# Kernel tuning notes

Measured on AMD Instinct MI355X. Metric: run time of the kernel, lower is better.

Reference implementation:

```python
import jax, jax.numpy as jnp
import numpy as np

B, T, N, C = 4, 2048, 8, 64
HEADS, HEAD_DIM, V_UNIT, EMBED = 8, 64, 64, 64  # N*C == HEADS*HEAD_DIM == 512


def setup_inputs() -> dict:
    key = jax.random.key(0)
    ks = jax.random.split(key, 6)
    return {
        "values": jax.random.normal(ks[0], (B, T, N, C), dtype=jnp.float32),
        "keys": jax.random.normal(ks[1], (B, T, N, C), dtype=jnp.float32),
        "queries": jax.random.normal(ks[2], (B, T, N, C), dtype=jnp.float32),
        "Wq": jax.random.normal(ks[3], (HEADS * HEAD_DIM, N * C), dtype=jnp.float32) * 0.02,
        "W_fc": jax.random.normal(ks[4], (EMBED, EMBED), dtype=jnp.float32) * 0.02,
        "b_fc": jax.random.normal(ks[5], (EMBED,), dtype=jnp.float32) * 0.02,
    }


def reference(values, keys, queries, Wq, W_fc, b_fc):
    b, t, n, c = queries.shape
    atten_dim = t  # temporal mode
    # queries: flatten N*C, project, split heads -> [B, T, H, Dh]
    q = queries.reshape(b, atten_dim, n * c) @ Wq.T
    q = q.reshape(b, atten_dim, HEADS, HEAD_DIM)
    # keys/values: only reshaped in the original forward (their Linears are unused)
    k = keys.reshape(b, atten_dim, HEADS, HEAD_DIM)
    v = values.reshape(b, atten_dim, HEADS, V_UNIT)
    # energy: [B, Tq, Tk, H]
    energy = jnp.einsum("bqhd,bkhd->bqkh", q, k)
    # diagonal-exclusion mask applied additively BEFORE scaling (as in source)
    diag = jnp.eye(atten_dim, dtype=bool)[None, :, :, None]
    energy = jnp.where(diag, jnp.float32(-1e9), energy)
    attention = jax.nn.softmax(energy / jnp.sqrt(jnp.float32(HEAD_DIM)), axis=2)
    out = jnp.einsum("bqkh,bkhd->bqhd", attention, v)  # [B, T, H, Dv]
    out = out @ W_fc.T + b_fc
    return out
```

## Files before the change

kernel.cpp:

```cpp
#include <hip/hip_runtime.h>
#include <math.h>

#define BB 4
#define TT 2048
#define NH 8
#define HD 64
#define EMB 512

typedef unsigned short u16;
typedef short short8 __attribute__((ext_vector_type(8)));
typedef float f32x4 __attribute__((ext_vector_type(4)));
typedef float f32x16 __attribute__((ext_vector_type(16)));

#define MFMA32(a,b,c) __builtin_amdgcn_mfma_f32_32x32x16_bf16((a),(b),(c),0,0,0)
#define ZERO16 (f32x16){0.f,0.f,0.f,0.f,0.f,0.f,0.f,0.f,0.f,0.f,0.f,0.f,0.f,0.f,0.f,0.f}
#define QSCALE 0.1803368801111f

#if __has_builtin(__builtin_amdgcn_exp2f)
#define EXP2(x) __builtin_amdgcn_exp2f(x)
#else
#define EXP2(x) exp2f(x)
#endif

__device__ __forceinline__ float hi_part(float a) {
    return __uint_as_float(__float_as_uint(a) & 0xffff0000u);
}
__device__ __forceinline__ unsigned pack_hi2(float a, float b) {
    return (__float_as_uint(a) >> 16) | (__float_as_uint(b) & 0xffff0000u);
}
__device__ __forceinline__ unsigned pack_lo2(float a, float b) {
    return pack_hi2(a - hi_part(a), b - hi_part(b));
}
__device__ __forceinline__ unsigned rne1(float x) {
    unsigned u = __float_as_uint(x);
    return (u + 0x7fffu + ((u >> 16) & 1u)) >> 16;
}
__device__ __forceinline__ unsigned rne2(float a, float b) {
    return rne1(a) | (rne1(b) << 16);
}
__device__ __forceinline__ void gl_lds16(const u16* g, void* l) {
    __builtin_amdgcn_global_load_lds(
        (const __attribute__((address_space(1))) unsigned int*)g,
        (__attribute__((address_space(3))) unsigned int*)l, 16, 0, 0);
}

__global__ __launch_bounds__(256, 3) void prep(
        const float* __restrict__ Aq, const float* __restrict__ Wq,
        const float* __restrict__ K,  const float* __restrict__ V,
        const float* __restrict__ Wfc,
        u16* __restrict__ Qh, u16* __restrict__ Ql,
        u16* __restrict__ Kh, u16* __restrict__ Vh,
        u16* __restrict__ Wh, u16* __restrict__ Wl) {
    __shared__ __align__(16) unsigned char sm[49152];
    const int tid = threadIdx.x;

    if (blockIdx.x < 512) {
        const int AoffH = 0, AoffL = 16384, BoffH = 32768, BoffL = 40960;
        const int lane = tid & 63, w = tid >> 6;
        const int l31 = lane & 31, hh2 = lane >> 5;
        const int qb = (blockIdx.x & 63) * 128, ob = (blockIdx.x >> 6) * 64;
        const int ar = tid >> 1, ahalf = tid & 1;
        const int br = tid >> 2, bq = tid & 3;

        const float* ap = Aq + (size_t)(qb + ar) * EMB + ahalf * 32;
        const float* bp = Wq + (size_t)(ob + br) * EMB + bq * 16;

        float4 a4[8], b4[4];
        #pragma unroll
        for (int c = 0; c < 8; c++) a4[c] = *(const float4*)(ap + 4*c);
        #pragma unroll
        for (int c = 0; c < 4; c++) b4[c] = *(const float4*)(bp + 4*c);

        f32x16 acc[2] = {ZERO16, ZERO16};

        for (int k0 = 0; k0 < EMB; k0 += 64) {
            __syncthreads();
            #pragma unroll
            for (int c = 0; c < 4; c++) {
                float4 f0 = a4[2*c], f1 = a4[2*c+1];
                uint4 hh = make_uint4(pack_hi2(f0.x,f0.y), pack_hi2(f0.z,f0.w),
                                      pack_hi2(f1.x,f1.y), pack_hi2(f1.z,f1.w));
                uint4 ll = make_uint4(pack_lo2(f0.x,f0.y), pack_lo2(f0.z,f0.w),
                                      pack_lo2(f1.x,f1.y), pack_lo2(f1.z,f1.w));
                const int phys = ((ahalf*4 + c) ^ (ar & 7)) * 16;
                *(uint4*)(sm + AoffH + ar*128 + phys) = hh;
                *(uint4*)(sm + AoffL + ar*128 + phys) = ll;
            }
            #pragma unroll
            for (int c = 0; c < 2; c++) {
                float4 f0 = b4[2*c], f1 = b4[2*c+1];
                uint4 hh = make_uint4(pack_hi2(f0.x,f0.y), pack_hi2(f0.z,f0.w),
                                      pack_hi2(f1.x,f1.y), pack_hi2(f1.z,f1.w));
                uint4 ll = make_uint4(pack_lo2(f0.x,f0.y), pack_lo2(f0.z,f0.w),
                                      pack_lo2(f1.x,f1.y), pack_lo2(f1.z,f1.w));
                const int phys = ((bq*2 + c) ^ (br & 7)) * 16;
                *(uint4*)(sm + BoffH + br*128 + phys) = hh;
                *(uint4*)(sm + BoffL + br*128 + phys) = ll;
            }
            if (k0 + 64 < EMB) {
                #pragma unroll
                for (int c = 0; c < 8; c++) a4[c] = *(const float4*)(ap + k0 + 64 + 4*c);
                #pragma unroll
                for (int c = 0; c < 4; c++) b4[c] = *(const float4*)(bp + k0 + 64 + 4*c);
            }
            __syncthreads();

            const unsigned char* arow = sm + (w*32 + l31) * 128;
            #pragma unroll
            for (int ks = 0; ks < 4; ks++) {
                const int co = (((ks*2 + hh2) ^ (l31 & 7)) * 16);
                short8 ah = *(const short8*)(arow + AoffH + co);
                short8 al = *(const short8*)(arow + AoffL + co);
                #pragma unroll
                for (int nb = 0; nb < 2; nb++) {
                    const unsigned char* brow = sm + (nb*32 + l31) * 128 + co;
                    short8 bh = *(const short8*)(brow + BoffH);
                    short8 bl = *(const short8*)(brow + BoffL);
                    acc[nb] = MFMA32(ah, bh, acc[nb]);
                    acc[nb] = MFMA32(al, bh, acc[nb]);
                    acc[nb] = MFMA32(ah, bl, acc[nb]);
                }
            }
        }

        __syncthreads();
        float* Ls = (float*)sm;
        #pragma unroll
        for (int nb = 0; nb < 2; nb++)
            #pragma unroll
            for (int rg = 0; rg < 16; rg++) {
                const int row = w*32 + (rg & 3) + 8*(rg >> 2) + 4*hh2;
                Ls[row*68 + nb*32 + l31] = acc[nb][rg] * QSCALE;
            }
        const int q = w*32 + (lane >> 1), o0 = (lane & 1) * 32;
        float v[32];
        #pragma unroll
        for (int j = 0; j < 8; j++) {
            f32x4 t = *(const f32x4*)(Ls + q*68 + o0 + 4*j);
            v[4*j]=t[0]; v[4*j+1]=t[1]; v[4*j+2]=t[2]; v[4*j+3]=t[3];
        }
        u16* qd = Qh + (size_t)(qb + q) * EMB + ob + o0;
        u16* ql = Ql + (size_t)(qb + q) * EMB + ob + o0;
        #pragma unroll
        for (int c = 0; c < 4; c++) {
            uint4 hh = make_uint4(pack_hi2(v[8*c],v[8*c+1]), pack_hi2(v[8*c+2],v[8*c+3]),
                                  pack_hi2(v[8*c+4],v[8*c+5]), pack_hi2(v[8*c+6],v[8*c+7]));
            uint4 ll = make_uint4(pack_lo2(v[8*c],v[8*c+1]), pack_lo2(v[8*c+2],v[8*c+3]),
                                  pack_lo2(v[8*c+4],v[8*c+5]), pack_lo2(v[8*c+6],v[8*c+7]));
            *(uint4*)(qd + 8*c) = hh;
            *(uint4*)(ql + 8*c) = ll;
        }
    } else {
        const int u = blockIdx.x - 512;
        const int kt0 = (u & 31) * 64, h = (u >> 5) & 7, b = u >> 8;
        float (*Vf)[68] = (float(*)[68])sm;
        const int t = tid >> 2, c0 = (tid & 3) * 16;
        {
            const float* kp = K + ((size_t)(b*TT + kt0 + t)) * EMB + h*HD + c0;
            float v[16];
            #pragma unroll
            for (int j = 0; j < 4; j++) {
                float4 f = *(const float4*)(kp + 4*j);
                v[4*j]=f.x; v[4*j+1]=f.y; v[4*j+2]=f.z; v[4*j+3]=f.w;
            }
            u16* kd = Kh + ((size_t)(b*NH + h)*TT + kt0 + t)*HD;
            #pragma unroll
            for (int half = 0; half < 2; half++) {
                const int phys = ((c0 >> 3) + half) ^ (t & 7);
                unsigned hh[4];
                #pragma unroll
                for (int j = 0; j < 4; j++)
                    hh[j] = rne2(v[half*8 + 2*j], v[half*8 + 2*j + 1]);
                *(uint4*)(kd + phys*8) = make_uint4(hh[0],hh[1],hh[2],hh[3]);
            }
        }
        {
            const float* vp = V + ((size_t)(b*TT + kt0 + t)) * EMB + h*HD + c0;
            #pragma unroll
            for (int j = 0; j < 4; j++)
                *(float4*)&Vf[t][c0 + 4*j] = *(const float4*)(vp + 4*j);
        }
        __syncthreads();
        {
            const int d = tid >> 2, t0 = (tid & 3) * 16;
            float v[16];
            #pragma unroll
            for (int i = 0; i < 16; i++) v[i] = Vf[t0 + i][d];
            u16* vd = Vh + (((size_t)(b*NH + h)*32 + (kt0 >> 6))*64 + d)*64;
            #pragma unroll
            for (int half = 0; half < 2; half++) {
                const int phys = ((t0 >> 3) + half) ^ (d & 7);
                unsigned hh[4];
                #pragma unroll
                for (int j = 0; j < 4; j++)
                    hh[j] = rne2(v[half*8 + 2*j], v[half*8 + 2*j + 1]);
                *(uint4*)(vd + phys*8) = make_uint4(hh[0],hh[1],hh[2],hh[3]);
            }
        }
        if (u == 0) {
            const int i0 = tid * 16;
            float v[16];
            #pragma unroll
            for (int j = 0; j < 4; j++) {
                float4 f = *(const float4*)(Wfc + i0 + 4*j);
                v[4*j]=f.x; v[4*j+1]=f.y; v[4*j+2]=f.z; v[4*j+3]=f.w;
            }
            unsigned hh[8], ll[8];
            #pragma unroll
            for (int j = 0; j < 8; j++) {
                hh[j] = pack_hi2(v[2*j], v[2*j+1]);
                ll[j] = pack_lo2(v[2*j], v[2*j+1]);
            }
            *(uint4*)(Wh + i0)     = make_uint4(hh[0],hh[1],hh[2],hh[3]);
            *(uint4*)(Wh + i0 + 8) = make_uint4(hh[4],hh[5],hh[6],hh[7]);
            *(uint4*)(Wl + i0)     = make_uint4(ll[0],ll[1],ll[2],ll[3]);
            *(uint4*)(Wl + i0 + 8) = make_uint4(ll[4],ll[5],ll[6],ll[7]);
        }
    }
}

__global__ __launch_bounds__(256, 3) void attn_v6(
        const u16* __restrict__ Qh, const u16* __restrict__ Ql,
        const u16* __restrict__ Kh, const u16* __restrict__ Vh,
        const u16* __restrict__ Wh, const u16* __restrict__ Wl,
        const float* __restrict__ bfc, float* __restrict__ out) {
    __shared__ __align__(16) unsigned char sm[49152];

    const int tid = threadIdx.x, lane = tid & 63, w = tid >> 6;
    const int l31 = lane & 31, hh2 = lane >> 5;
    const int s = l31 & 7, s0 = s & 1, t3 = s >> 1;
    const int qb = blockIdx.x * 128, h = blockIdx.y, b = blockIdx.z;
    const int qg = qb + w*32 + l31;
    const int rowoff = l31 * 128;

    int fo[4];
    #pragma unroll
    for (int f = 0; f < 4; f++)
        fo[f] = ((f ^ t3) << 5) | ((hh2 ^ s0) << 4);

    const size_t qo = ((size_t)(b*TT + qg)) * EMB + h*HD + hh2*8;
    short8 qfh[4], qfl[4];
    #pragma unroll
    for (int f = 0; f < 4; f++) {
        qfh[f] = *(const short8*)(Qh + qo + 16*f);
        qfl[f] = *(const short8*)(Ql + qo + 16*f);
    }

    const size_t bh = (size_t)(b*NH + h) * TT * HD;
    const u16* ssrc = ((w < 2) ? (Kh + bh) : (Vh + bh)) + (w & 1) * 2048;
    const int sdst = ((w >= 2) ? 8192 : 0) + (w & 1) * 4096;

    #pragma unroll
    for (int i = 0; i < 4; i++)
        gl_lds16(ssrc + i*512 + lane*8, sm + sdst + i*1024);
    __syncthreads();

    f32x16 co[2] = {ZERO16, ZERO16};
    float lsum = 0.f;
    const int diagTile = (qb >> 6) + (w >> 1);
    const int Poff = 32768 + w * 4096;

    for (int kt = 0; kt < 32; kt++) {
        const int cb = (kt & 1) * 16384;
        if (kt < 31) {
            const u16* src2 = ssrc + (size_t)(kt + 1) * 4096;
            unsigned char* dst2 = sm + (16384 - cb) + sdst;
            #pragma unroll
            for (int i = 0; i < 4; i++)
                gl_lds16(src2 + i*512 + lane*8, dst2 + i*1024);
        }

        f32x16 sc[2];
        #pragma unroll
        for (int kc = 0; kc < 2; kc++) {
            const unsigned char* kb = sm + cb + kc*4096 + rowoff;
            f32x16 c = ZERO16;
            #pragma unroll
            for (int f = 0; f < 4; f++) {
                short8 ah = *(const short8*)(kb + fo[f]);
                c = MFMA32(ah, qfh[f], c);
                c = MFMA32(ah, qfl[f], c);
            }
            sc[kc] = c;
        }

        if (kt == diagTile) {
            const int local = qg & 63;
            if (((local >> 2) & 1) == hh2) {
                const int reg = (local & 3) + ((local >> 3) & 3) * 4;
                if (local < 32) sc[0][reg] = -1e30f;
                else            sc[1][reg] = -1e30f;
            }
        }

        #pragma unroll
        for (int kc = 0; kc < 2; kc++)
            #pragma unroll
            for (int e = 0; e < 16; e++) {
                float p = EXP2(sc[kc][e]);
                sc[kc][e] = p;
                lsum += p;
            }

        #pragma unroll
        for (int kc = 0; kc < 2; kc++)
            #pragma unroll
            for (int rg = 0; rg < 4; rg++) {
                uint2 hh = make_uint2(pack_hi2(sc[kc][rg*4+0], sc[kc][rg*4+1]),
                                      pack_hi2(sc[kc][rg*4+2], sc[kc][rg*4+3]));
                *(uint2*)(sm + Poff + rowoff +
                          ((((kc*4 + rg) ^ s) << 4) + (hh2 << 3))) = hh;
            }

        short8 pb[4];
        #pragma unroll
        for (int f = 0; f < 4; f++)
            pb[f] = *(const short8*)(sm + Poff + rowoff + fo[f]);
        #pragma unroll
        for (int m = 0; m < 2; m++) {
            const unsigned char* vb = sm + cb + 8192 + m*4096 + rowoff;
            #pragma unroll
            for (int f = 0; f < 4; f++) {
                short8 vh = *(const short8*)(vb + fo[f]);
                co[m] = MFMA32(vh, pb[f], co[m]);
            }
        }
        __syncthreads();
    }

    lsum += __shfl_xor(lsum, 32, 64);
    const float rl = 1.f / lsum;
    const int aOffH = w * 4096, aOffL = 16384 + w * 4096;
    #pragma unroll
    for (int m = 0; m < 2; m++)
        #pragma unroll
        for (int rg = 0; rg < 4; rg++) {
            float a0 = co[m][rg*4+0]*rl, a1 = co[m][rg*4+1]*rl;
            float a2 = co[m][rg*4+2]*rl, a3 = co[m][rg*4+3]*rl;
            uint2 hh = make_uint2(pack_hi2(a0,a1), pack_hi2(a2,a3));
            uint2 ll = make_uint2(pack_lo2(a0,a1), pack_lo2(a2,a3));
            const int off = rowoff + ((((m*4 + rg) ^ s) << 4) + (hh2 << 3));
            *(uint2*)(sm + aOffH + off) = hh;
            *(uint2*)(sm + aOffL + off) = ll;
        }
    short8 abh[4], abl[4];
    #pragma unroll
    for (int f = 0; f < 4; f++) {
        abh[f] = *(const short8*)(sm + aOffH + rowoff + fo[f]);
        abl[f] = *(const short8*)(sm + aOffL + rowoff + fo[f]);
    }
    f32x16 cf[2] = {ZERO16, ZERO16};
    #pragma unroll
    for (int eh = 0; eh < 2; eh++) {
        const u16* wp  = Wh + (eh*32 + l31)*HD + hh2*8;
        const u16* wpl = Wl + (eh*32 + l31)*HD + hh2*8;
        #pragma unroll
        for (int f = 0; f < 4; f++) {
            short8 whv = *(const short8*)(wp + 16*f);
            cf[eh] = MFMA32(whv, abh[f], cf[eh]);
        }
        #pragma unroll
        for (int f = 0; f < 4; f++) {
            short8 wlv = *(const short8*)(wpl + 16*f);
            cf[eh] = MFMA32(wlv, abh[f], cf[eh]);
        }
        #pragma unroll
        for (int f = 0; f < 4; f++) {
            short8 whv = *(const short8*)(wp + 16*f);
            cf[eh] = MFMA32(whv, abl[f], cf[eh]);
        }
    }
    __syncthreads();
    float* Ls = (float*)sm;
    #pragma unroll
    for (int eh = 0; eh < 2; eh++)
        #pragma unroll
        for (int rg = 0; rg < 4; rg++) {
            const int e0 = eh*32 + rg*8 + hh2*4;
            *(f32x4*)(Ls + (w*32 + l31)*72 + e0) =
                (f32x4){cf[eh][rg*4+0], cf[eh][rg*4+1], cf[eh][rg*4+2], cf[eh][rg*4+3]};
        }
    const int q2 = w*32 + (lane >> 1), e0s = (lane & 1) * 32;
    const float* lrow = Ls + q2*72 + e0s;
    float* orow = out + ((size_t)((b*TT + qb + q2)*NH + h))*HD + e0s;
    #pragma unroll
    for (int j = 0; j < 8; j++) {
        f32x4 v = *(const f32x4*)(lrow + 4*j);
        float4 bv = *(const float4*)(bfc + e0s + 4*j);
        *(float4*)(orow + 4*j) = make_float4(v[0]+bv.x, v[1]+bv.y, v[2]+bv.z, v[3]+bv.w);
    }
}

__global__ __launch_bounds__(256) void qproj_f32(const float* __restrict__ A,
                                                 const float* __restrict__ W,
                                                 float* __restrict__ Q) {
    __shared__ float As[16][68];
    __shared__ float Ws[16][68];
    const int tid = threadIdx.x;
    const int bm = blockIdx.x * 64, bo = blockIdx.y * 64;
    const int tx = tid & 15, ty = tid >> 4;
    const int lm = tid >> 2, lk = (tid & 3) * 4;
    float acc[4][4] = {};
    for (int k0 = 0; k0 < EMB; k0 += 16) {
        float4 a4 = *(const float4*)(A + (size_t)(bm + lm) * EMB + k0 + lk);
        float4 w4 = *(const float4*)(W + (size_t)(bo + lm) * EMB + k0 + lk);
        As[lk+0][lm]=a4.x; As[lk+1][lm]=a4.y; As[lk+2][lm]=a4.z; As[lk+3][lm]=a4.w;
        Ws[lk+0][lm]=w4.x; Ws[lk+1][lm]=w4.y; Ws[lk+2][lm]=w4.z; Ws[lk+3][lm]=w4.w;
        __syncthreads();
        #pragma unroll
        for (int k = 0; k < 16; k++) {
            float a[4], ww[4];
            #pragma unroll
            for (int i = 0; i < 4; i++) a[i] = As[k][ty*4+i];
            #pragma unroll
            for (int j = 0; j < 4; j++) ww[j] = Ws[k][tx*4+j];
            #pragma unroll
            for (int i = 0; i < 4; i++)
                #pragma unroll
                for (int j = 0; j < 4; j++) acc[i][j] = fmaf(a[i], ww[j], acc[i][j]);
        }
        __syncthreads();
    }
    #pragma unroll
    for (int i = 0; i < 4; i++)
        #pragma unroll
        for (int j = 0; j < 4; j++)
            Q[(size_t)(bm + ty*4 + i) * EMB + bo + tx*4 + j] = acc[i][j];
}

__device__ __forceinline__ float rdlane(float v, int l) {
    return __uint_as_float(__builtin_amdgcn_readlane(__float_as_uint(v), l));
}

__global__ __launch_bounds__(256) void attn_valu(const float* __restrict__ qws,
                                                 const float* __restrict__ keys,
                                                 const float* __restrict__ values,
                                                 const float* __restrict__ Wfc,
                                                 const float* __restrict__ bfc,
                                                 float* __restrict__ out) {
    __shared__ float Kt[64][65];
    __shared__ float Vt[64][65];
    __shared__ float Wfs[64][64];
    __shared__ float bfs[64];
    const int tid = threadIdx.x, lane = tid & 63, wave = tid >> 6;
    const int h = blockIdx.y, b = blockIdx.z;
    const int rowBase = blockIdx.x * 32 + wave * 8;
    #pragma unroll
    for (int rep = 0; rep < 4; rep++) {
        int e4 = rep * 256 + tid;
        int e = e4 >> 4, d = (e4 & 15) * 4;
        float4 w4 = *(const float4*)(Wfc + e * 64 + d);
        Wfs[d+0][e]=w4.x; Wfs[d+1][e]=w4.y; Wfs[d+2][e]=w4.z; Wfs[d+3][e]=w4.w;
    }
    if (tid < 64) bfs[tid] = bfc[tid];
    float qreg[8];
    #pragma unroll
    for (int r = 0; r < 8; r++)
        qreg[r] = qws[(((size_t)b * TT + rowBase + r) * NH + h) * HD + lane];
    float m[8], lsum[8], acc[8];
    #pragma unroll
    for (int r = 0; r < 8; r++) { m[r] = -INFINITY; lsum[r] = 0.f; acc[r] = 0.f; }
    const float* kbase = keys   + ((size_t)b * TT * NH + h) * HD;
    const float* vbase = values + ((size_t)b * TT * NH + h) * HD;
    for (int kt0 = 0; kt0 < TT; kt0 += 64) {
        __syncthreads();
        #pragma unroll
        for (int rep = 0; rep < 4; rep++) {
            int e4 = rep * 256 + tid;
            int kr = e4 >> 4, d = (e4 & 15) * 4;
            size_t g = ((size_t)(kt0 + kr) * NH) * HD + d;
            float4 k4 = *(const float4*)(kbase + g);
            float4 v4 = *(const float4*)(vbase + g);
            Kt[kr][d+0]=k4.x; Kt[kr][d+1]=k4.y; Kt[kr][d+2]=k4.z; Kt[kr][d+3]=k4.w;
            Vt[kr][d+0]=v4.x; Vt[kr][d+1]=v4.y; Vt[kr][d+2]=v4.z; Vt[kr][d+3]=v4.w;
        }
        __syncthreads();
        float en[8];
        #pragma unroll
        for (int r = 0; r < 8; r++) en[r] = 0.f;
        #pragma unroll 16
        for (int d = 0; d < 64; d++) {
            float kv = Kt[lane][d];
            #pragma unroll
            for (int r = 0; r < 8; r++) en[r] = fmaf(rdlane(qreg[r], d), kv, en[r]);
        }
        const int key = kt0 + lane;
        float p[8], alph[8];
        #pragma unroll
        for (int r = 0; r < 8; r++) {
            float e = en[r];
            if (key == rowBase + r) e = -1e9f;
            e *= 0.125f;
            float tm = e;
            #pragma unroll
            for (int ss = 32; ss > 0; ss >>= 1) tm = fmaxf(tm, __shfl_xor(tm, ss, 64));
            float mn = fmaxf(m[r], tm);
            float pvv = __expf(e - mn);
            float ps = pvv;
            #pragma unroll
            for (int ss = 32; ss > 0; ss >>= 1) ps += __shfl_xor(ps, ss, 64);
            alph[r] = __expf(m[r] - mn);
            m[r] = mn;
            lsum[r] = lsum[r] * alph[r] + ps;
            p[r] = pvv;
        }
        #pragma unroll
        for (int r = 0; r < 8; r++) acc[r] *= alph[r];
        #pragma unroll 16
        for (int j = 0; j < 64; j++) {
            float vv = Vt[j][lane];
            #pragma unroll
            for (int r = 0; r < 8; r++) acc[r] = fmaf(rdlane(p[r], j), vv, acc[r]);
        }
    }
    #pragma unroll
    for (int r = 0; r < 8; r++) {
        float a = acc[r] / lsum[r];
        float o = bfs[lane];
        #pragma unroll 16
        for (int d = 0; d < 64; d++) o = fmaf(rdlane(a, d), Wfs[d][lane], o);
        out[(((size_t)b * TT + rowBase + r) * NH + h) * HD + lane] = o;
    }
}

extern "C" void kernel_launch(void* const* d_in, const int* in_sizes, int n_in,
                              void* d_out, int out_size, void* d_ws, size_t ws_size,
                              hipStream_t stream) {
    const float* values  = (const float*)d_in[0];
    const float* keys    = (const float*)d_in[1];
    const float* queries = (const float*)d_in[2];
    const float* Wq      = (const float*)d_in[3];
    const float* Wfc     = (const float*)d_in[4];
    const float* bfc     = (const float*)d_in[5];
    float* out = (float*)d_out;

    const size_t NE = (size_t)BB * TT * EMB;
    const size_t need = (4 * NE + 2 * 4096) * sizeof(u16);
    if (ws_size >= need) {
        u16* Qh = (u16*)d_ws;
        u16* Ql = Qh + NE;
        u16* Kh = Qh + 2*NE;
        u16* Vh = Qh + 3*NE;
        u16* Wh = Qh + 4*NE;
        u16* Wl = Wh + 4096;
        prep<<<1536, 256, 0, stream>>>(queries, Wq, keys, values, Wfc,
                                       Qh, Ql, Kh, Vh, Wh, Wl);
        attn_v6<<<dim3(TT/128, NH, BB), 256, 0, stream>>>(Qh, Ql, Kh, Vh,
                                                          Wh, Wl, bfc, out);
    } else {
        float* qws = (float*)d_ws;
        qproj_f32<<<dim3((BB*TT)/64, EMB/64), 256, 0, stream>>>(queries, Wq, qws);
        attn_valu<<<dim3(TT/32, NH, BB), 256, 0, stream>>>(qws, keys, values, Wfc, bfc, out);
    }
}
```

Baseline: 180.1 us.

## Split prep into Q-projection and K/V conversion kernels, RNE-round P

```diff
diff --git a/kernel.cpp b/kernel.cpp
--- a/kernel.cpp
+++ b/kernel.cpp
@@ -44,182 +44,187 @@
         (__attribute__((address_space(3))) unsigned int*)l, 16, 0, 0);
 }
 
-__global__ __launch_bounds__(256, 3) void prep(
-        const float* __restrict__ Aq, const float* __restrict__ Wq,
-        const float* __restrict__ K,  const float* __restrict__ V,
-        const float* __restrict__ Wfc,
-        u16* __restrict__ Qh, u16* __restrict__ Ql,
-        u16* __restrict__ Kh, u16* __restrict__ Vh,
-        u16* __restrict__ Wh, u16* __restrict__ Wl) {
+__global__ __launch_bounds__(256, 3) void qproj_pf(const float* __restrict__ Aq,
+                                                   const float* __restrict__ Wq,
+                                                   u16* __restrict__ Qh,
+                                                   u16* __restrict__ Ql) {
     __shared__ __align__(16) unsigned char sm[49152];
+    const int AoffH = 0, AoffL = 16384, BoffH = 32768, BoffL = 40960;
     const int tid = threadIdx.x;
-
-    if (blockIdx.x < 512) {
-        const int AoffH = 0, AoffL = 16384, BoffH = 32768, BoffL = 40960;
-        const int lane = tid & 63, w = tid >> 6;
-        const int l31 = lane & 31, hh2 = lane >> 5;
-        const int qb = (blockIdx.x & 63) * 128, ob = (blockIdx.x >> 6) * 64;
-        const int ar = tid >> 1, ahalf = tid & 1;
-        const int br = tid >> 2, bq = tid & 3;
-
-        const float* ap = Aq + (size_t)(qb + ar) * EMB + ahalf * 32;
-        const float* bp = Wq + (size_t)(ob + br) * EMB + bq * 16;
-
-        float4 a4[8], b4[4];
-        #pragma unroll
-        for (int c = 0; c < 8; c++) a4[c] = *(const float4*)(ap + 4*c);
-        #pragma unroll
-        for (int c = 0; c < 4; c++) b4[c] = *(const float4*)(bp + 4*c);
-
-        f32x16 acc[2] = {ZERO16, ZERO16};
-
-        for (int k0 = 0; k0 < EMB; k0 += 64) {
-            __syncthreads();
-            #pragma unroll
-            for (int c = 0; c < 4; c++) {
-                float4 f0 = a4[2*c], f1 = a4[2*c+1];
-                uint4 hh = make_uint4(pack_hi2(f0.x,f0.y), pack_hi2(f0.z,f0.w),
-                                      pack_hi2(f1.x,f1.y), pack_hi2(f1.z,f1.w));
-                uint4 ll = make_uint4(pack_lo2(f0.x,f0.y), pack_lo2(f0.z,f0.w),
-                                      pack_lo2(f1.x,f1.y), pack_lo2(f1.z,f1.w));
-                const int phys = ((ahalf*4 + c) ^ (ar & 7)) * 16;
-                *(uint4*)(sm + AoffH + ar*128 + phys) = hh;
-                *(uint4*)(sm + AoffL + ar*128 + phys) = ll;
+    const int lane = tid & 63, w = tid >> 6;
+    const int l31 = lane & 31, hh2 = lane >> 5;
+    const int qb = (blockIdx.x & 63) * 128, ob = (blockIdx.x >> 6) * 64;
+    const int ar = tid >> 1, ahalf = tid & 1;
+    const int br = tid >> 2, bq = tid & 3;
+
+    const float* ap = Aq + (size_t)(qb + ar) * EMB + ahalf * 32;
+    const float* bp = Wq + (size_t)(ob + br) * EMB + bq * 16;
+
+    float4 a4[8], b4[4];
+    #pragma unroll
+    for (int c = 0; c < 8; c++) a4[c] = *(const float4*)(ap + 4*c);
+    #pragma unroll
+    for (int c = 0; c < 4; c++) b4[c] = *(const float4*)(bp + 4*c);
+
+    f32x16 acc[2] = {ZERO16, ZERO16};
+
+    for (int k0 = 0; k0 < EMB; k0 += 64) {
+        __syncthreads();
+        #pragma unroll
+        for (int c = 0; c < 4; c++) {
+            float4 f0 = a4[2*c], f1 = a4[2*c+1];
+            uint4 hh = make_uint4(pack_hi2(f0.x,f0.y), pack_hi2(f0.z,f0.w),
+                                  pack_hi2(f1.x,f1.y), pack_hi2(f1.z,f1.w));
+            uint4 ll = make_uint4(pack_lo2(f0.x,f0.y), pack_lo2(f0.z,f0.w),
+                                  pack_lo2(f1.x,f1.y), pack_lo2(f1.z,f1.w));
+            const int phys = ((ahalf*4 + c) ^ (ar & 7)) * 16;
+            *(uint4*)(sm + AoffH + ar*128 + phys) = hh;
+            *(uint4*)(sm + AoffL + ar*128 + phys) = ll;
+        }
+        #pragma unroll
+        for (int c = 0; c < 2; c++) {
+            float4 f0 = b4[2*c], f1 = b4[2*c+1];
+            uint4 hh = make_uint4(pack_hi2(f0.x,f0.y), pack_hi2(f0.z,f0.w),
+                                  pack_hi2(f1.x,f1.y), pack_hi2(f1.z,f1.w));
+            uint4 ll = make_uint4(pack_lo2(f0.x,f0.y), pack_lo2(f0.z,f0.w),
+                                  pack_lo2(f1.x,f1.y), pack_lo2(f1.z,f1.w));
+            const int phys = ((bq*2 + c) ^ (br & 7)) * 16;
+            *(uint4*)(sm + BoffH + br*128 + phys) = hh;
+            *(uint4*)(sm + BoffL + br*128 + phys) = ll;
+        }
+        if (k0 + 64 < EMB) {
+            #pragma unroll
+            for (int c = 0; c < 8; c++) a4[c] = *(const float4*)(ap + k0 + 64 + 4*c);
+            #pragma unroll
+            for (int c = 0; c < 4; c++) b4[c] = *(const float4*)(bp + k0 + 64 + 4*c);
+        }
+        __syncthreads();
+
+        const unsigned char* arow = sm + (w*32 + l31) * 128;
+        #pragma unroll
+        for (int ks = 0; ks < 4; ks++) {
+            const int co = (((ks*2 + hh2) ^ (l31 & 7)) * 16);
+            short8 ah = *(const short8*)(arow + AoffH + co);
+            short8 al = *(const short8*)(arow + AoffL + co);
+            #pragma unroll
+            for (int nb = 0; nb < 2; nb++) {
+                const unsigned char* brow = sm + (nb*32 + l31) * 128 + co;
+                short8 bh = *(const short8*)(brow + BoffH);
+                short8 bl = *(const short8*)(brow + BoffL);
+                acc[nb] = MFMA32(ah, bh, acc[nb]);
+                acc[nb] = MFMA32(al, bh, acc[nb]);
+                acc[nb] = MFMA32(ah, bl, acc[nb]);
             }
-            #pragma unroll
-            for (int c = 0; c < 2; c++) {
-                float4 f0 = b4[2*c], f1 = b4[2*c+1];
-                uint4 hh = make_uint4(pack_hi2(f0.x,f0.y), pack_hi2(f0.z,f0.w),
-                                      pack_hi2(f1.x,f1.y), pack_hi2(f1.z,f1.w));
-                uint4 ll = make_uint4(pack_lo2(f0.x,f0.y), pack_lo2(f0.z,f0.w),
-                                      pack_lo2(f1.x,f1.y), pack_lo2(f1.z,f1.w));
-                const int phys = ((bq*2 + c) ^ (br & 7)) * 16;
-                *(uint4*)(sm + BoffH + br*128 + phys) = hh;
-                *(uint4*)(sm + BoffL + br*128 + phys) = ll;
-            }
-            if (k0 + 64 < EMB) {
-                #pragma unroll
-                for (int c = 0; c < 8; c++) a4[c] = *(const float4*)(ap + k0 + 64 + 4*c);
-                #pragma unroll
-                for (int c = 0; c < 4; c++) b4[c] = *(const float4*)(bp + k0 + 64 + 4*c);
-            }
-            __syncthreads();
-
-            const unsigned char* arow = sm + (w*32 + l31) * 128;
-            #pragma unroll
-            for (int ks = 0; ks < 4; ks++) {
-                const int co = (((ks*2 + hh2) ^ (l31 & 7)) * 16);
-                short8 ah = *(const short8*)(arow + AoffH + co);
-                short8 al = *(const short8*)(arow + AoffL + co);
-                #pragma unroll
-                for (int nb = 0; nb < 2; nb++) {
-                    const unsigned char* brow = sm + (nb*32 + l31) * 128 + co;
-                    short8 bh = *(const short8*)(brow + BoffH);
-                    short8 bl = *(const short8*)(brow + BoffL);
-                    acc[nb] = MFMA32(ah, bh, acc[nb]);
-                    acc[nb] = MFMA32(al, bh, acc[nb]);
-                    acc[nb] = MFMA32(ah, bl, acc[nb]);
-                }
-            }
-        }
-
-        __syncthreads();
-        float* Ls = (float*)sm;
-        #pragma unroll
-        for (int nb = 0; nb < 2; nb++)
-            #pragma unroll
-            for (int rg = 0; rg < 16; rg++) {
-                const int row = w*32 + (rg & 3) + 8*(rg >> 2) + 4*hh2;
-                Ls[row*68 + nb*32 + l31] = acc[nb][rg] * QSCALE;
-            }
-        const int q = w*32 + (lane >> 1), o0 = (lane & 1) * 32;
-        float v[32];
+        }
+    }
+
+    __syncthreads();
+    float* Ls = (float*)sm;
+    #pragma unroll
+    for (int nb = 0; nb < 2; nb++)
+        #pragma unroll
+        for (int rg = 0; rg < 16; rg++) {
+            const int row = w*32 + (rg & 3) + 8*(rg >> 2) + 4*hh2;
+            Ls[row*68 + nb*32 + l31] = acc[nb][rg] * QSCALE;
+        }
+    const int q = w*32 + (lane >> 1), o0 = (lane & 1) * 32;
+    float v[32];
+    #pragma unroll
+    for (int j = 0; j < 8; j++) {
+        f32x4 t = *(const f32x4*)(Ls + q*68 + o0 + 4*j);
+        v[4*j]=t[0]; v[4*j+1]=t[1]; v[4*j+2]=t[2]; v[4*j+3]=t[3];
+    }
+    u16* qd = Qh + (size_t)(qb + q) * EMB + ob + o0;
+    u16* ql = Ql + (size_t)(qb + q) * EMB + ob + o0;
+    #pragma unroll
+    for (int c = 0; c < 4; c++) {
+        uint4 hh = make_uint4(pack_hi2(v[8*c],v[8*c+1]), pack_hi2(v[8*c+2],v[8*c+3]),
+                              pack_hi2(v[8*c+4],v[8*c+5]), pack_hi2(v[8*c+6],v[8*c+7]));
+        uint4 ll = make_uint4(pack_lo2(v[8*c],v[8*c+1]), pack_lo2(v[8*c+2],v[8*c+3]),
+                              pack_lo2(v[8*c+4],v[8*c+5]), pack_lo2(v[8*c+6],v[8*c+7]));
+        *(uint4*)(qd + 8*c) = hh;
+        *(uint4*)(ql + 8*c) = ll;
+    }
+}
+
+__global__ __launch_bounds__(256) void convert2(const float* __restrict__ K,
+                                                const float* __restrict__ V,
+                                                const float* __restrict__ Wfc,
+                                                u16* __restrict__ Kh,
+                                                u16* __restrict__ Vh,
+                                                u16* __restrict__ Wh,
+                                                u16* __restrict__ Wl) {
+    const int x = blockIdx.x;
+    const int c8 = x & 7, h = (x >> 3) & 7, b = x >> 6;
+    const int tbase = c8 * 256;
+    const int tid = threadIdx.x, lane = tid & 63, w = tid >> 6;
+
+    const int c0 = (tid & 3) * 16;
+    #pragma unroll
+    for (int it = 0; it < 4; it++) {
+        const int t = tbase + it*64 + (tid >> 2);
+        const float* kp = K + ((size_t)(b*TT + t)) * EMB + h*HD + c0;
+        float v[16];
+        #pragma unroll
+        for (int j = 0; j < 4; j++) {
+            float4 f = *(const float4*)(kp + 4*j);
+            v[4*j]=f.x; v[4*j+1]=f.y; v[4*j+2]=f.z; v[4*j+3]=f.w;
+        }
+        u16* kd = Kh + ((size_t)(b*NH + h)*TT + t)*HD;
+        #pragma unroll
+        for (int half = 0; half < 2; half++) {
+            const int phys = ((c0 >> 3) + half) ^ (t & 7);
+            unsigned hh[4];
+            #pragma unroll
+            for (int j = 0; j < 4; j++)
+                hh[j] = rne2(v[half*8 + 2*j], v[half*8 + 2*j + 1]);
+            *(uint4*)(kd + phys*8) = make_uint4(hh[0],hh[1],hh[2],hh[3]);
+        }
+    }
+
+    const int d = lane;
+    const int tile = c8*4 + w;
+    const float* vcol = V + ((size_t)(b*TT + tile*64)) * EMB + h*HD + d;
+    u16* vd = Vh + (((size_t)(b*NH + h)*32 + tile)*64 + d)*64;
+    #pragma unroll
+    for (int tc = 0; tc < 4; tc++) {
+        float vv[16];
+        #pragma unroll
+        for (int i = 0; i < 16; i++)
+            vv[i] = vcol[(size_t)(tc*16 + i) * EMB];
+        #pragma unroll
+        for (int half = 0; half < 2; half++) {
+            const int phys = (tc*2 + half) ^ (d & 7);
+            unsigned hh[4];
+            #pragma unroll
+            for (int j = 0; j < 4; j++)
+                hh[j] = rne2(vv[half*8 + 2*j], vv[half*8 + 2*j + 1]);
+            *(uint4*)(vd + phys*8) = make_uint4(hh[0],hh[1],hh[2],hh[3]);
+        }
+    }
+
+    if (x == 0) {
+        const int i0 = tid * 16;
+        float v[16];
+        #pragma unroll
+        for (int j = 0; j < 4; j++) {
+            float4 f = *(const float4*)(Wfc + i0 + 4*j);
+            v[4*j]=f.x; v[4*j+1]=f.y; v[4*j+2]=f.z; v[4*j+3]=f.w;
+        }
+        unsigned hh[8], ll[8];
         #pragma unroll
         for (int j = 0; j < 8; j++) {
-            f32x4 t = *(const f32x4*)(Ls + q*68 + o0 + 4*j);
-            v[4*j]=t[0]; v[4*j+1]=t[1]; v[4*j+2]=t[2]; v[4*j+3]=t[3];
-        }
-        u16* qd = Qh + (size_t)(qb + q) * EMB + ob + o0;
-        u16* ql = Ql + (size_t)(qb + q) * EMB + ob + o0;
-        #pragma unroll
-        for (int c = 0; c < 4; c++) {
-            uint4 hh = make_uint4(pack_hi2(v[8*c],v[8*c+1]), pack_hi2(v[8*c+2],v[8*c+3]),
-                                  pack_hi2(v[8*c+4],v[8*c+5]), pack_hi2(v[8*c+6],v[8*c+7]));
-            uint4 ll = make_uint4(pack_lo2(v[8*c],v[8*c+1]), pack_lo2(v[8*c+2],v[8*c+3]),
-                                  pack_lo2(v[8*c+4],v[8*c+5]), pack_lo2(v[8*c+6],v[8*c+7]));
-            *(uint4*)(qd + 8*c) = hh;
-            *(uint4*)(ql + 8*c) = ll;
-        }
-    } else {
-        const int u = blockIdx.x - 512;
-        const int kt0 = (u & 31) * 64, h = (u >> 5) & 7, b = u >> 8;
-        float (*Vf)[68] = (float(*)[68])sm;
-        const int t = tid >> 2, c0 = (tid & 3) * 16;
-        {
-            const float* kp = K + ((size_t)(b*TT + kt0 + t)) * EMB + h*HD + c0;
-            float v[16];
-            #pragma unroll
-            for (int j = 0; j < 4; j++) {
-                float4 f = *(const float4*)(kp + 4*j);
-                v[4*j]=f.x; v[4*j+1]=f.y; v[4*j+2]=f.z; v[4*j+3]=f.w;
-            }
-            u16* kd = Kh + ((size_t)(b*NH + h)*TT + kt0 + t)*HD;
-            #pragma unroll
-            for (int half = 0; half < 2; half++) {
-                const int phys = ((c0 >> 3) + half) ^ (t & 7);
-                unsigned hh[4];
-                #pragma unroll
-                for (int j = 0; j < 4; j++)
-                    hh[j] = rne2(v[half*8 + 2*j], v[half*8 + 2*j + 1]);
-                *(uint4*)(kd + phys*8) = make_uint4(hh[0],hh[1],hh[2],hh[3]);
-            }
-        }
-        {
-            const float* vp = V + ((size_t)(b*TT + kt0 + t)) * EMB + h*HD + c0;
-            #pragma unroll
-            for (int j = 0; j < 4; j++)
-                *(float4*)&Vf[t][c0 + 4*j] = *(const float4*)(vp + 4*j);
-        }
-        __syncthreads();
-        {
-            const int d = tid >> 2, t0 = (tid & 3) * 16;
-            float v[16];
-            #pragma unroll
-            for (int i = 0; i < 16; i++) v[i] = Vf[t0 + i][d];
-            u16* vd = Vh + (((size_t)(b*NH + h)*32 + (kt0 >> 6))*64 + d)*64;
-            #pragma unroll
-            for (int half = 0; half < 2; half++) {
-                const int phys = ((t0 >> 3) + half) ^ (d & 7);
-                unsigned hh[4];
-                #pragma unroll
-                for (int j = 0; j < 4; j++)
-                    hh[j] = rne2(v[half*8 + 2*j], v[half*8 + 2*j + 1]);
-                *(uint4*)(vd + phys*8) = make_uint4(hh[0],hh[1],hh[2],hh[3]);
-            }
-        }
-        if (u == 0) {
-            const int i0 = tid * 16;
-            float v[16];
-            #pragma unroll
-            for (int j = 0; j < 4; j++) {
-                float4 f = *(const float4*)(Wfc + i0 + 4*j);
-                v[4*j]=f.x; v[4*j+1]=f.y; v[4*j+2]=f.z; v[4*j+3]=f.w;
-            }
-            unsigned hh[8], ll[8];
-            #pragma unroll
-            for (int j = 0; j < 8; j++) {
-                hh[j] = pack_hi2(v[2*j], v[2*j+1]);
-                ll[j] = pack_lo2(v[2*j], v[2*j+1]);
-            }
-            *(uint4*)(Wh + i0)     = make_uint4(hh[0],hh[1],hh[2],hh[3]);
-            *(uint4*)(Wh + i0 + 8) = make_uint4(hh[4],hh[5],hh[6],hh[7]);
-            *(uint4*)(Wl + i0)     = make_uint4(ll[0],ll[1],ll[2],ll[3]);
-            *(uint4*)(Wl + i0 + 8) = make_uint4(ll[4],ll[5],ll[6],ll[7]);
-        }
-    }
-}
-
-__global__ __launch_bounds__(256, 3) void attn_v6(
+            hh[j] = pack_hi2(v[2*j], v[2*j+1]);
+            ll[j] = pack_lo2(v[2*j], v[2*j+1]);
+        }
+        *(uint4*)(Wh + i0)     = make_uint4(hh[0],hh[1],hh[2],hh[3]);
+        *(uint4*)(Wh + i0 + 8) = make_uint4(hh[4],hh[5],hh[6],hh[7]);
+        *(uint4*)(Wl + i0)     = make_uint4(ll[0],ll[1],ll[2],ll[3]);
+        *(uint4*)(Wl + i0 + 8) = make_uint4(ll[4],ll[5],ll[6],ll[7]);
+    }
+}
+
+__global__ __launch_bounds__(256, 3) void attn_v6b(
         const u16* __restrict__ Qh, const u16* __restrict__ Ql,
         const u16* __restrict__ Kh, const u16* __restrict__ Vh,
         const u16* __restrict__ Wh, const u16* __restrict__ Wl,
@@ -306,8 +311,8 @@
         for (int kc = 0; kc < 2; kc++)
             #pragma unroll
             for (int rg = 0; rg < 4; rg++) {
-                uint2 hh = make_uint2(pack_hi2(sc[kc][rg*4+0], sc[kc][rg*4+1]),
-                                      pack_hi2(sc[kc][rg*4+2], sc[kc][rg*4+3]));
+                uint2 hh = make_uint2(rne2(sc[kc][rg*4+0], sc[kc][rg*4+1]),
+                                      rne2(sc[kc][rg*4+2], sc[kc][rg*4+3]));
                 *(uint2*)(sm + Poff + rowoff +
                           ((((kc*4 + rg) ^ s) << 4) + (hh2 << 3))) = hh;
             }
@@ -543,10 +548,10 @@
         u16* Vh = Qh + 3*NE;
         u16* Wh = Qh + 4*NE;
         u16* Wl = Wh + 4096;
-        prep<<<1536, 256, 0, stream>>>(queries, Wq, keys, values, Wfc,
-                                       Qh, Ql, Kh, Vh, Wh, Wl);
-        attn_v6<<<dim3(TT/128, NH, BB), 256, 0, stream>>>(Qh, Ql, Kh, Vh,
-                                                          Wh, Wl, bfc, out);
+        qproj_pf<<<512, 256, 0, stream>>>(queries, Wq, Qh, Ql);
+        convert2<<<256, 256, 0, stream>>>(keys, values, Wfc, Kh, Vh, Wh, Wl);
+        attn_v6b<<<dim3(TT/128, NH, BB), 256, 0, stream>>>(Qh, Ql, Kh, Vh,
+                                                           Wh, Wl, bfc, out);
     } else {
         float* qws = (float*)d_ws;
         qproj_f32<<<dim3((BB*TT)/64, EMB/64), 256, 0, stream>>>(queries, Wq, qws);
```

After: 195.2 us. +8.4%, slower.
